# Performance work log

Hardware: AMD Instinct MI355X
Metric: run time of the kernel (lower is better)

Reference implementation:

```python
import jax, jax.numpy as jnp
import numpy as np

B, F, E = 1024, 128, 256
HEAD_NUM = 8
USE_RES = True
SCALING = False


def setup_inputs() -> dict:
    key = jax.random.key(0)
    k_in, kq, kk, kv, kr = jax.random.split(key, 5)
    std = 0.05  # matches nn.init.normal_(std=0.05)
    return {
        "inputs": jax.random.normal(k_in, (B, F, E), dtype=jnp.float32),
        "W_Query": jax.random.normal(kq, (E, E), dtype=jnp.float32) * std,
        "W_key": jax.random.normal(kk, (E, E), dtype=jnp.float32) * std,
        "W_Value": jax.random.normal(kv, (E, E), dtype=jnp.float32) * std,
        "W_Res": jax.random.normal(kr, (E, E), dtype=jnp.float32) * std,
    }


def reference(inputs, W_Query, W_key, W_Value, W_Res):
    b, f, e = inputs.shape
    h = HEAD_NUM
    d = e // h  # att_embedding_size
    # QKV projections; split(dim=2)+stack == reshape to (b, f, h, d)
    q = jnp.einsum('bfe,eo->bfo', inputs, W_Query).reshape(b, f, h, d)
    k = jnp.einsum('bfe,eo->bfo', inputs, W_key).reshape(b, f, h, d)
    v = jnp.einsum('bfe,eo->bfo', inputs, W_Value).reshape(b, f, h, d)
    # attention scores per head: [b, h, f, f]
    scores = jnp.einsum('bihd,bjhd->bhij', q, k)
    if SCALING:
        scores = scores / jnp.sqrt(jnp.asarray(d, scores.dtype))
    attn = jax.nn.softmax(scores, axis=-1)
    # weighted values; cat(split(result,1), -1) == reshape heads back to E in order
    out = jnp.einsum('bhij,bjhd->bihd', attn, v).reshape(b, f, e)
    if USE_RES:
        out = out + jnp.einsum('bfe,eo->bfo', inputs, W_Res)
    return jax.nn.relu(out)
```

## Files before the change

### kernel.cpp

```cpp
#include <hip/hip_runtime.h>
#include <hip/hip_bf16.h>

#define B_SZ 1024
#define F_SZ 128
#define E_SZ 256
#define H_NUM 8
#define D_SZ 32

typedef __bf16 bf16x8 __attribute__((ext_vector_type(8)));
typedef float f32x4 __attribute__((ext_vector_type(4)));
typedef unsigned short u16x4 __attribute__((ext_vector_type(4)));

__device__ __forceinline__ bf16x8 frag_at(const __hip_bfloat16* p) {
  return *reinterpret_cast<const bf16x8*>(p);
}

__device__ __forceinline__ bf16x8 pack_bf16x8(float4 a, float4 b) {
  bf16x8 r;
  r[0] = (__bf16)a.x; r[1] = (__bf16)a.y; r[2] = (__bf16)a.z; r[3] = (__bf16)a.w;
  r[4] = (__bf16)b.x; r[5] = (__bf16)b.y; r[6] = (__bf16)b.z; r[7] = (__bf16)b.w;
  return r;
}

__global__ void transpose_weights(const float* __restrict__ W0,
                                  const float* __restrict__ W1,
                                  const float* __restrict__ W2,
                                  const float* __restrict__ W3,
                                  __hip_bfloat16* __restrict__ WT) {
  __shared__ float tile[64][65];
  const int wsel = blockIdx.x >> 4;
  const float* W = wsel == 0 ? W0 : wsel == 1 ? W1 : wsel == 2 ? W2 : W3;
  __hip_bfloat16* T = WT + wsel * (E_SZ * E_SZ);
  const int t = blockIdx.x & 15;
  const int tr = (t >> 2) * 64, tc = (t & 3) * 64;
  for (int k = 0; k < 16; ++k) {
    int fl = k * 256 + threadIdx.x;
    int lr = fl >> 6, lc = fl & 63;
    tile[lr][lc] = W[(tr + lr) * E_SZ + tc + lc];
  }
  __syncthreads();
  for (int k = 0; k < 16; ++k) {
    int fl = k * 256 + threadIdx.x;
    int lr = fl >> 6, lc = fl & 63;
    T[(tc + lr) * E_SZ + tr + lc] = __float2bfloat16(tile[lc][lr]);
  }
}

#define XST 264
#define QST 40
#define VST 136
#define PST 136

#define XS_OFF 0
#define QS_OFF (128 * XST)
#define KS_OFF (QS_OFF + 128 * QST)
#define RS_OFF (KS_OFF + 128 * QST)
#define VT_OFF (RS_OFF + 128 * QST)
#define PS_OFF (VT_OFF + 32 * VST)
#define SMEM_ELEMS (PS_OFF + 8 * 16 * PST)

__global__ __launch_bounds__(512, 2)
void fused_attn(const float* __restrict__ X,
                const __hip_bfloat16* __restrict__ WT,
                float* __restrict__ out) {
  __shared__ __align__(16) __hip_bfloat16 smem[SMEM_ELEMS];
  __hip_bfloat16* const Xs = smem + XS_OFF;
  __hip_bfloat16* const Qs = smem + QS_OFF;
  __hip_bfloat16* const Ks = smem + KS_OFF;
  __hip_bfloat16* const Rs = smem + RS_OFF;
  __hip_bfloat16* const Vt = smem + VT_OFF;
  __hip_bfloat16* const Ps = smem + PS_OFF;

  const int tid  = threadIdx.x;
  const int wave = tid >> 6;
  const int lane = tid & 63;
  const int quad = lane >> 4;
  const int l16  = lane & 15;
  const int b    = blockIdx.x;

  const float* Xb = X + (size_t)b * (F_SZ * E_SZ);
  #pragma unroll
  for (int i = 0; i < 8; ++i) {
    int ch = i * 512 + tid;
    int r = ch >> 5, c = ch & 31;
    const float* sa = Xb + r * E_SZ + c * 8;
    float4 a0 = *reinterpret_cast<const float4*>(sa);
    float4 a1 = *reinterpret_cast<const float4*>(sa + 4);
    *reinterpret_cast<bf16x8*>(&Xs[r * XST + c * 8]) = pack_bf16x8(a0, a1);
  }
  __syncthreads();

  const int pmat = wave >> 1;
  const int prh  = wave & 1;
  const __hip_bfloat16* Wmat = WT + pmat * (E_SZ * E_SZ);
  __hip_bfloat16* const Pw = Ps + wave * 16 * PST;

  for (int h = 0; h < H_NUM; ++h) {
    {
      const __hip_bfloat16* Wh = Wmat + (h * D_SZ) * E_SZ;
      f32x4 acc[4][2];
      #pragma unroll
      for (int mt = 0; mt < 4; ++mt) {
        acc[mt][0] = f32x4{0.f, 0.f, 0.f, 0.f};
        acc[mt][1] = f32x4{0.f, 0.f, 0.f, 0.f};
      }
      #pragma unroll
      for (int ks = 0; ks < 8; ++ks) {
        const int ko = ks * 32 + quad * 8;
        bf16x8 b0 = frag_at(Wh + l16 * E_SZ + ko);
        bf16x8 b1 = frag_at(Wh + (16 + l16) * E_SZ + ko);
        #pragma unroll
        for (int mt = 0; mt < 4; ++mt) {
          bf16x8 af = frag_at(&Xs[(prh * 64 + mt * 16 + l16) * XST + ko]);
          acc[mt][0] = __builtin_amdgcn_mfma_f32_16x16x32_bf16(af, b0, acc[mt][0], 0, 0, 0);
          acc[mt][1] = __builtin_amdgcn_mfma_f32_16x16x32_bf16(af, b1, acc[mt][1], 0, 0, 0);
        }
      }
      if (pmat == 2) {
        #pragma unroll
        for (int mt = 0; mt < 4; ++mt)
          #pragma unroll
          for (int nt = 0; nt < 2; ++nt) {
            u16x4 pk;
            #pragma unroll
            for (int reg = 0; reg < 4; ++reg) {
              __hip_bfloat16 bv = __float2bfloat16(acc[mt][nt][reg]);
              pk[reg] = *reinterpret_cast<unsigned short*>(&bv);
            }
            *reinterpret_cast<u16x4*>(
                &Vt[(nt * 16 + l16) * VST + prh * 64 + mt * 16 + quad * 4]) = pk;
          }
      } else {
        __hip_bfloat16* T = (pmat == 0) ? Qs : (pmat == 1) ? Ks : Rs;
        #pragma unroll
        for (int mt = 0; mt < 4; ++mt)
          #pragma unroll
          for (int nt = 0; nt < 2; ++nt)
            #pragma unroll
            for (int reg = 0; reg < 4; ++reg)
              T[(prh * 64 + mt * 16 + quad * 4 + reg) * QST + nt * 16 + l16] =
                  __float2bfloat16(acc[mt][nt][reg]);
      }
    }
    __syncthreads();

    {
      bf16x8 aq = frag_at(&Qs[(wave * 16 + l16) * QST + quad * 8]);
      f32x4 s[8];
      #pragma unroll
      for (int nt = 0; nt < 8; ++nt) {
        bf16x8 bk = frag_at(&Ks[(nt * 16 + l16) * QST + quad * 8]);
        s[nt] = __builtin_amdgcn_mfma_f32_16x16x32_bf16(
            aq, bk, f32x4{0.f, 0.f, 0.f, 0.f}, 0, 0, 0);
      }
      #pragma unroll
      for (int reg = 0; reg < 4; ++reg) {
        float m = s[0][reg];
        #pragma unroll
        for (int nt = 1; nt < 8; ++nt) m = fmaxf(m, s[nt][reg]);
        #pragma unroll
        for (int off = 8; off >= 1; off >>= 1) m = fmaxf(m, __shfl_xor(m, off));
        float sum = 0.f;
        #pragma unroll
        for (int nt = 0; nt < 8; ++nt) {
          float e = __expf(s[nt][reg] - m);
          s[nt][reg] = e;
          sum += e;
        }
        #pragma unroll
        for (int off = 8; off >= 1; off >>= 1) sum += __shfl_xor(sum, off);
        float inv = 1.f / sum;
        int r = quad * 4 + reg;
        #pragma unroll
        for (int nt = 0; nt < 8; ++nt)
          Pw[r * PST + nt * 16 + l16] = __float2bfloat16(s[nt][reg] * inv);
      }
    }

    {
      f32x4 o[2];
      o[0] = f32x4{0.f, 0.f, 0.f, 0.f};
      o[1] = f32x4{0.f, 0.f, 0.f, 0.f};
      #pragma unroll
      for (int ks = 0; ks < 4; ++ks) {
        const int ko = ks * 32 + quad * 8;
        bf16x8 ap  = *reinterpret_cast<const bf16x8*>(Pw + l16 * PST + ko);
        bf16x8 bv0 = frag_at(&Vt[l16 * VST + ko]);
        bf16x8 bv1 = frag_at(&Vt[(16 + l16) * VST + ko]);
        o[0] = __builtin_amdgcn_mfma_f32_16x16x32_bf16(ap, bv0, o[0], 0, 0, 0);
        o[1] = __builtin_amdgcn_mfma_f32_16x16x32_bf16(ap, bv1, o[1], 0, 0, 0);
      }
      #pragma unroll
      for (int nt = 0; nt < 2; ++nt)
        #pragma unroll
        for (int reg = 0; reg < 4; ++reg) {
          int f = wave * 16 + quad * 4 + reg;
          float rv = (float)Rs[f * QST + nt * 16 + l16];
          float v = o[nt][reg] + rv;
          size_t idx = ((size_t)b * F_SZ + f) * E_SZ + h * D_SZ + nt * 16 + l16;
          out[idx] = (v < 0.f) ? 0.f : v;
        }
    }
    __syncthreads();
  }
}

extern "C" void kernel_launch(void* const* d_in, const int* in_sizes, int n_in,
                              void* d_out, int out_size, void* d_ws, size_t ws_size,
                              hipStream_t stream) {
  const float* X  = (const float*)d_in[0];
  const float* Wq = (const float*)d_in[1];
  const float* Wk = (const float*)d_in[2];
  const float* Wv = (const float*)d_in[3];
  const float* Wr = (const float*)d_in[4];
  float* out = (float*)d_out;

  __hip_bfloat16* WT = (__hip_bfloat16*)d_ws;

  (void)hipGetLastError();
  transpose_weights<<<64, 256, 0, stream>>>(Wq, Wk, Wv, Wr, WT);
  fused_attn<<<B_SZ, 512, 0, stream>>>(X, WT, out);

  hipError_t err = hipGetLastError();
  if (err != hipSuccess) {
    hipMemsetAsync(d_out, 0x7F, 1024, stream);
  }
}
```

Before: 428.8 us.

## Precompute bf16 X globally, drop X LDS tile, transpose MFMA operands for vector stores

Adds a separate kernel that converts X to bf16 in workspace, and the fused kernel now reads X fragments straight from global memory instead of staging a padded 128x256 tile in LDS. Removing that tile shrinks shared memory, so launch bounds rise to 4 blocks per CU for higher occupancy. MFMA operand order is swapped so results are laid out transposed, which allows packed u16x4 LDS writes, a softmax that reduces across only two shuffle steps, and float4 output stores. The trade-off is an extra bf16 X write and read through global memory, and X fragments are re-read from global or L2 on every head iteration.

```diff
diff --git a/kernel.cpp b/kernel.cpp
--- a/kernel.cpp
+++ b/kernel.cpp
@@ -20,6 +20,17 @@
   r[0] = (__bf16)a.x; r[1] = (__bf16)a.y; r[2] = (__bf16)a.z; r[3] = (__bf16)a.w;
   r[4] = (__bf16)b.x; r[5] = (__bf16)b.y; r[6] = (__bf16)b.z; r[7] = (__bf16)b.w;
   return r;
+}
+
+__device__ __forceinline__ unsigned short f2bf_bits(float f) {
+  __hip_bfloat16 b = __float2bfloat16(f);
+  return *reinterpret_cast<unsigned short*>(&b);
+}
+
+__device__ __forceinline__ float bf_bits2f(unsigned short u) {
+  unsigned int x = ((unsigned int)u) << 16;
+  union { unsigned int i; float f; } c; c.i = x;
+  return c.f;
 }
 
 __global__ void transpose_weights(const float* __restrict__ W0,
@@ -46,25 +57,30 @@
   }
 }
 
-#define XST 264
+__global__ __launch_bounds__(256)
+void cvt_x(const float* __restrict__ X, __hip_bfloat16* __restrict__ Xb) {
+  size_t i = ((size_t)blockIdx.x * 256 + threadIdx.x) * 8;
+  float4 a0 = *reinterpret_cast<const float4*>(X + i);
+  float4 a1 = *reinterpret_cast<const float4*>(X + i + 4);
+  *reinterpret_cast<bf16x8*>(Xb + i) = pack_bf16x8(a0, a1);
+}
+
 #define QST 40
 #define VST 136
 #define PST 136
 
-#define XS_OFF 0
-#define QS_OFF (128 * XST)
-#define KS_OFF (QS_OFF + 128 * QST)
-#define RS_OFF (KS_OFF + 128 * QST)
-#define VT_OFF (RS_OFF + 128 * QST)
+#define QS_OFF 0
+#define KS_OFF (128 * QST)
+#define RS_OFF (2 * 128 * QST)
+#define VT_OFF (3 * 128 * QST)
 #define PS_OFF (VT_OFF + 32 * VST)
-#define SMEM_ELEMS (PS_OFF + 8 * 16 * PST)
-
-__global__ __launch_bounds__(512, 2)
-void fused_attn(const float* __restrict__ X,
+#define SMEM_ELEMS (PS_OFF + 128 * PST)
+
+__global__ __launch_bounds__(512, 4)
+void fused_attn(const __hip_bfloat16* __restrict__ Xb,
                 const __hip_bfloat16* __restrict__ WT,
                 float* __restrict__ out) {
   __shared__ __align__(16) __hip_bfloat16 smem[SMEM_ELEMS];
-  __hip_bfloat16* const Xs = smem + XS_OFF;
   __hip_bfloat16* const Qs = smem + QS_OFF;
   __hip_bfloat16* const Ks = smem + KS_OFF;
   __hip_bfloat16* const Rs = smem + RS_OFF;
@@ -77,103 +93,101 @@
   const int quad = lane >> 4;
   const int l16  = lane & 15;
   const int b    = blockIdx.x;
-
-  const float* Xb = X + (size_t)b * (F_SZ * E_SZ);
-  #pragma unroll
-  for (int i = 0; i < 8; ++i) {
-    int ch = i * 512 + tid;
-    int r = ch >> 5, c = ch & 31;
-    const float* sa = Xb + r * E_SZ + c * 8;
-    float4 a0 = *reinterpret_cast<const float4*>(sa);
-    float4 a1 = *reinterpret_cast<const float4*>(sa + 4);
-    *reinterpret_cast<bf16x8*>(&Xs[r * XST + c * 8]) = pack_bf16x8(a0, a1);
-  }
-  __syncthreads();
+  const int fw   = wave * 16;
 
   const int pmat = wave >> 1;
   const int prh  = wave & 1;
+  const __hip_bfloat16* Xw = Xb + ((size_t)b * F_SZ + prh * 64) * E_SZ;
   const __hip_bfloat16* Wmat = WT + pmat * (E_SZ * E_SZ);
-  __hip_bfloat16* const Pw = Ps + wave * 16 * PST;
+  __hip_bfloat16* const Pw = Ps + fw * PST;
 
   for (int h = 0; h < H_NUM; ++h) {
     {
       const __hip_bfloat16* Wh = Wmat + (h * D_SZ) * E_SZ;
-      f32x4 acc[4][2];
-      #pragma unroll
-      for (int mt = 0; mt < 4; ++mt) {
-        acc[mt][0] = f32x4{0.f, 0.f, 0.f, 0.f};
-        acc[mt][1] = f32x4{0.f, 0.f, 0.f, 0.f};
-      }
+      f32x4 acc[2][4];
+      #pragma unroll
+      for (int nt = 0; nt < 2; ++nt)
+        #pragma unroll
+        for (int mt = 0; mt < 4; ++mt) acc[nt][mt] = f32x4{0.f, 0.f, 0.f, 0.f};
+
       #pragma unroll
       for (int ks = 0; ks < 8; ++ks) {
         const int ko = ks * 32 + quad * 8;
-        bf16x8 b0 = frag_at(Wh + l16 * E_SZ + ko);
-        bf16x8 b1 = frag_at(Wh + (16 + l16) * E_SZ + ko);
+        bf16x8 aw0 = frag_at(Wh + l16 * E_SZ + ko);
+        bf16x8 aw1 = frag_at(Wh + (16 + l16) * E_SZ + ko);
         #pragma unroll
         for (int mt = 0; mt < 4; ++mt) {
-          bf16x8 af = frag_at(&Xs[(prh * 64 + mt * 16 + l16) * XST + ko]);
-          acc[mt][0] = __builtin_amdgcn_mfma_f32_16x16x32_bf16(af, b0, acc[mt][0], 0, 0, 0);
-          acc[mt][1] = __builtin_amdgcn_mfma_f32_16x16x32_bf16(af, b1, acc[mt][1], 0, 0, 0);
+          bf16x8 ax = frag_at(Xw + (mt * 16 + l16) * E_SZ + ko);
+          if (pmat != 2) {
+            acc[0][mt] = __builtin_amdgcn_mfma_f32_16x16x32_bf16(aw0, ax, acc[0][mt], 0, 0, 0);
+            acc[1][mt] = __builtin_amdgcn_mfma_f32_16x16x32_bf16(aw1, ax, acc[1][mt], 0, 0, 0);
+          } else {
+            acc[0][mt] = __builtin_amdgcn_mfma_f32_16x16x32_bf16(ax, aw0, acc[0][mt], 0, 0, 0);
+            acc[1][mt] = __builtin_amdgcn_mfma_f32_16x16x32_bf16(ax, aw1, acc[1][mt], 0, 0, 0);
+          }
         }
       }
-      if (pmat == 2) {
-        #pragma unroll
-        for (int mt = 0; mt < 4; ++mt)
+      if (pmat != 2) {
+        __hip_bfloat16* T = (pmat == 0) ? Qs : (pmat == 1) ? Ks : Rs;
+        #pragma unroll
+        for (int nt = 0; nt < 2; ++nt)
           #pragma unroll
-          for (int nt = 0; nt < 2; ++nt) {
+          for (int mt = 0; mt < 4; ++mt) {
             u16x4 pk;
             #pragma unroll
-            for (int reg = 0; reg < 4; ++reg) {
-              __hip_bfloat16 bv = __float2bfloat16(acc[mt][nt][reg]);
-              pk[reg] = *reinterpret_cast<unsigned short*>(&bv);
-            }
+            for (int reg = 0; reg < 4; ++reg) pk[reg] = f2bf_bits(acc[nt][mt][reg]);
+            *reinterpret_cast<u16x4*>(
+                &T[(prh * 64 + mt * 16 + l16) * QST + nt * 16 + quad * 4]) = pk;
+          }
+      } else {
+        #pragma unroll
+        for (int nt = 0; nt < 2; ++nt)
+          #pragma unroll
+          for (int mt = 0; mt < 4; ++mt) {
+            u16x4 pk;
+            #pragma unroll
+            for (int reg = 0; reg < 4; ++reg) pk[reg] = f2bf_bits(acc[nt][mt][reg]);
             *reinterpret_cast<u16x4*>(
                 &Vt[(nt * 16 + l16) * VST + prh * 64 + mt * 16 + quad * 4]) = pk;
           }
-      } else {
-        __hip_bfloat16* T = (pmat == 0) ? Qs : (pmat == 1) ? Ks : Rs;
-        #pragma unroll
-        for (int mt = 0; mt < 4; ++mt)
-          #pragma unroll
-          for (int nt = 0; nt < 2; ++nt)
-            #pragma unroll
-            for (int reg = 0; reg < 4; ++reg)
-              T[(prh * 64 + mt * 16 + quad * 4 + reg) * QST + nt * 16 + l16] =
-                  __float2bfloat16(acc[mt][nt][reg]);
       }
     }
     __syncthreads();
 
     {
-      bf16x8 aq = frag_at(&Qs[(wave * 16 + l16) * QST + quad * 8]);
+      bf16x8 bq = frag_at(&Qs[(fw + l16) * QST + quad * 8]);
       f32x4 s[8];
       #pragma unroll
       for (int nt = 0; nt < 8; ++nt) {
-        bf16x8 bk = frag_at(&Ks[(nt * 16 + l16) * QST + quad * 8]);
+        bf16x8 ak = frag_at(&Ks[(nt * 16 + l16) * QST + quad * 8]);
         s[nt] = __builtin_amdgcn_mfma_f32_16x16x32_bf16(
-            aq, bk, f32x4{0.f, 0.f, 0.f, 0.f}, 0, 0, 0);
-      }
-      #pragma unroll
-      for (int reg = 0; reg < 4; ++reg) {
-        float m = s[0][reg];
-        #pragma unroll
-        for (int nt = 1; nt < 8; ++nt) m = fmaxf(m, s[nt][reg]);
-        #pragma unroll
-        for (int off = 8; off >= 1; off >>= 1) m = fmaxf(m, __shfl_xor(m, off));
-        float sum = 0.f;
-        #pragma unroll
-        for (int nt = 0; nt < 8; ++nt) {
+            ak, bq, f32x4{0.f, 0.f, 0.f, 0.f}, 0, 0, 0);
+      }
+      float m = s[0][0];
+      #pragma unroll
+      for (int nt = 0; nt < 8; ++nt)
+        #pragma unroll
+        for (int reg = 0; reg < 4; ++reg) m = fmaxf(m, s[nt][reg]);
+      m = fmaxf(m, __shfl_xor(m, 16));
+      m = fmaxf(m, __shfl_xor(m, 32));
+      float sum = 0.f;
+      #pragma unroll
+      for (int nt = 0; nt < 8; ++nt)
+        #pragma unroll
+        for (int reg = 0; reg < 4; ++reg) {
           float e = __expf(s[nt][reg] - m);
           s[nt][reg] = e;
           sum += e;
         }
-        #pragma unroll
-        for (int off = 8; off >= 1; off >>= 1) sum += __shfl_xor(sum, off);
-        float inv = 1.f / sum;
-        int r = quad * 4 + reg;
-        #pragma unroll
-        for (int nt = 0; nt < 8; ++nt)
-          Pw[r * PST + nt * 16 + l16] = __float2bfloat16(s[nt][reg] * inv);
+      sum += __shfl_xor(sum, 16);
+      sum += __shfl_xor(sum, 32);
+      const float inv = 1.f / sum;
+      #pragma unroll
+      for (int nt = 0; nt < 8; ++nt) {
+        u16x4 pk;
+        #pragma unroll
+        for (int reg = 0; reg < 4; ++reg) pk[reg] = f2bf_bits(s[nt][reg] * inv);
+        *reinterpret_cast<u16x4*>(&Pw[l16 * PST + nt * 16 + quad * 4]) = pk;
       }
     }
 
@@ -184,22 +198,28 @@
       #pragma unroll
       for (int ks = 0; ks < 4; ++ks) {
         const int ko = ks * 32 + quad * 8;
-        bf16x8 ap  = *reinterpret_cast<const bf16x8*>(Pw + l16 * PST + ko);
-        bf16x8 bv0 = frag_at(&Vt[l16 * VST + ko]);
-        bf16x8 bv1 = frag_at(&Vt[(16 + l16) * VST + ko]);
-        o[0] = __builtin_amdgcn_mfma_f32_16x16x32_bf16(ap, bv0, o[0], 0, 0, 0);
-        o[1] = __builtin_amdgcn_mfma_f32_16x16x32_bf16(ap, bv1, o[1], 0, 0, 0);
-      }
-      #pragma unroll
-      for (int nt = 0; nt < 2; ++nt)
-        #pragma unroll
-        for (int reg = 0; reg < 4; ++reg) {
-          int f = wave * 16 + quad * 4 + reg;
-          float rv = (float)Rs[f * QST + nt * 16 + l16];
-          float v = o[nt][reg] + rv;
-          size_t idx = ((size_t)b * F_SZ + f) * E_SZ + h * D_SZ + nt * 16 + l16;
-          out[idx] = (v < 0.f) ? 0.f : v;
-        }
+        bf16x8 bp  = *reinterpret_cast<const bf16x8*>(Pw + l16 * PST + ko);
+        bf16x8 av0 = frag_at(&Vt[l16 * VST + ko]);
+        bf16x8 av1 = frag_at(&Vt[(16 + l16) * VST + ko]);
+        o[0] = __builtin_amdgcn_mfma_f32_16x16x32_bf16(av0, bp, o[0], 0, 0, 0);
+        o[1] = __builtin_amdgcn_mfma_f32_16x16x32_bf16(av1, bp, o[1], 0, 0, 0);
+      }
+      const size_t orow = ((size_t)b * F_SZ + fw + l16) * E_SZ + h * D_SZ;
+      #pragma unroll
+      for (int nt = 0; nt < 2; ++nt) {
+        u16x4 rv = *reinterpret_cast<const u16x4*>(
+            &Rs[(fw + l16) * QST + nt * 16 + quad * 4]);
+        float4 st;
+        float v0 = o[nt][0] + bf_bits2f(rv[0]);
+        float v1 = o[nt][1] + bf_bits2f(rv[1]);
+        float v2 = o[nt][2] + bf_bits2f(rv[2]);
+        float v3 = o[nt][3] + bf_bits2f(rv[3]);
+        st.x = (v0 < 0.f) ? 0.f : v0;
+        st.y = (v1 < 0.f) ? 0.f : v1;
+        st.z = (v2 < 0.f) ? 0.f : v2;
+        st.w = (v3 < 0.f) ? 0.f : v3;
+        *reinterpret_cast<float4*>(&out[orow + nt * 16 + quad * 4]) = st;
+      }
     }
     __syncthreads();
   }
@@ -215,11 +235,14 @@
   const float* Wr = (const float*)d_in[4];
   float* out = (float*)d_out;
 
-  __hip_bfloat16* WT = (__hip_bfloat16*)d_ws;
+  char* ws = (char*)d_ws;
+  __hip_bfloat16* WT = (__hip_bfloat16*)ws;
+  __hip_bfloat16* Xb = (__hip_bfloat16*)(ws + 512 * 1024);
 
   (void)hipGetLastError();
   transpose_weights<<<64, 256, 0, stream>>>(Wq, Wk, Wv, Wr, WT);
-  fused_attn<<<B_SZ, 512, 0, stream>>>(X, WT, out);
+  cvt_x<<<(B_SZ * F_SZ * E_SZ / 8) / 256, 256, 0, stream>>>(X, Xb);
+  fused_attn<<<B_SZ, 512, 0, stream>>>(Xb, WT, out);
 
   hipError_t err = hipGetLastError();
   if (err != hipSuccess) {
```

After: 555.6 us. 29.6% more time.
